# Kernel optimization log

Measured on AMD Instinct MI355X. Metric: run time of the kernel, lower is better.

The kernel has to match this reference:

```python
import jax, jax.numpy as jnp
import numpy as np

N = 100_000      # n_nodes
DEG = 32         # edge_threshold (fixed out-degree)
D = 64           # in_channels = out_channels, heads = 1
NEG_SLOPE = 0.2


def setup_inputs() -> dict:
    key = jax.random.key(0)
    k1, k2, k3, k4 = jax.random.split(key, 4)
    x = jax.random.normal(k1, (N, D), jnp.float32)
    # fixed-degree edge list with no self loops (offset in [1, N-1])
    src = jnp.repeat(jnp.arange(N, dtype=jnp.int64), DEG)
    off = jax.random.randint(k2, (N * DEG,), 1, N, dtype=jnp.int64)
    dst = (src + off) % N
    edge_index = jnp.stack([src, dst])  # [2, E]
    # glorot init as in the torch module
    stdv_w = float(np.sqrt(6.0 / (D + D)))
    weight = jax.random.uniform(k3, (D, D), jnp.float32, -stdv_w, stdv_w)
    stdv_a = float(np.sqrt(6.0 / (1 + 2 * D)))  # att is [1, heads=1, 2*D]
    att = jax.random.uniform(k4, (2 * D,), jnp.float32, -stdv_a, stdv_a)
    bias = jnp.zeros((D,), jnp.float32)
    return {"x": x, "edge_index": edge_index, "weight": weight, "att": att, "bias": bias}


def reference(x, edge_index, weight, att, bias):
    n, d = x.shape
    h = x @ weight                               # [N, D] (heads=1)
    # add self loops (inputs are constructed without self loops)
    loop = jnp.arange(n, dtype=edge_index.dtype)
    src = jnp.concatenate([edge_index[0], loop])  # message sources (x_j)
    dst = jnp.concatenate([edge_index[1], loop])  # aggregation targets (x_i)
    # GAT edge score: (cat([x_i, x_j]) * att).sum(-1) = h_i@a_i + h_j@a_j
    a_i, a_j = att[:d], att[d:]
    s_i = h @ a_i                                 # [N]
    s_j = h @ a_j                                 # [N]
    alpha = s_i[dst] + s_j[src]                   # [E+N]
    alpha = jnp.where(alpha > 0, alpha, NEG_SLOPE * alpha)  # leaky_relu
    # segment softmax over destination nodes (numerically stable)
    amax = jax.ops.segment_max(alpha, dst, num_segments=n)
    e = jnp.exp(alpha - amax[dst])
    denom = jax.ops.segment_sum(e, dst, num_segments=n)
    w = e / (denom[dst] + 1e-16)                  # [E+N]
    # weighted scatter-add aggregation of source features
    out = jax.ops.segment_sum(h[src] * w[:, None], dst, num_segments=n)  # [N, D]
    out = out + bias                              # head-mean is identity (heads=1)
    # dropout(p=0.5) is identity in eval mode; F.normalize (L2, dim=1, eps=1e-12)
    norm = jnp.linalg.norm(out, axis=1, keepdims=True)
    return out / jnp.maximum(norm, 1e-12)
```

## Files before the change

kernel.cpp:

```cpp
#include <hip/hip_runtime.h>
#include <math.h>

#define NEG_SLOPE 0.2f
#define PCHUNK 4096
#define NBINS_MAX 392
#define BIN_EDGE_CAP 8704

__device__ __forceinline__ unsigned pk_bf16x2(float a, float b) {
    unsigned ua = __float_as_uint(a);
    ua = (ua + 0x7FFFu + ((ua >> 16) & 1u)) >> 16;
    unsigned ub = __float_as_uint(b);
    ub = (ub + 0x7FFFu + ((ub >> 16) & 1u)) & 0xFFFF0000u;
    return ua | ub;
}

__global__ __launch_bounds__(256) void k_linear(const float* __restrict__ x,
        const float* __restrict__ W, const float* __restrict__ att,
        uint2* __restrict__ h16, float* __restrict__ si, float* __restrict__ sj,
        int n)
{
    int tid = threadIdx.x;
    int lane = tid & 63;
    int wv = tid >> 6;
    int q = lane >> 4;
    int f = lane & 15;

    const float4* W4 = (const float4*)W;
    float4 Wr[16];
#pragma unroll
    for (int kb = 0; kb < 16; ++kb)
        Wr[kb] = W4[(16 * q + kb) * 16 + f];

    const float4* att4 = (const float4*)att;
    float4 ai4 = att4[f];
    float4 aj4 = att4[16 + f];
    const float4* x4 = (const float4*)x;

    int row0 = (blockIdx.x * 4 + wv) * 8;
    for (int r = 0; r < 8; ++r) {
        int row = row0 + r;
        if (row >= n) break;
        size_t xb = (size_t)row * 16 + 4 * q;
        float4 xq0 = x4[xb + 0];
        float4 xq1 = x4[xb + 1];
        float4 xq2 = x4[xb + 2];
        float4 xq3 = x4[xb + 3];
        float4 acc = {0.f, 0.f, 0.f, 0.f};
#define LSTEP(xc, kb) { float4 w4 = Wr[kb]; \
        acc.x = fmaf((xc), w4.x, acc.x); acc.y = fmaf((xc), w4.y, acc.y); \
        acc.z = fmaf((xc), w4.z, acc.z); acc.w = fmaf((xc), w4.w, acc.w); }
        LSTEP(xq0.x, 0)  LSTEP(xq0.y, 1)  LSTEP(xq0.z, 2)  LSTEP(xq0.w, 3)
        LSTEP(xq1.x, 4)  LSTEP(xq1.y, 5)  LSTEP(xq1.z, 6)  LSTEP(xq1.w, 7)
        LSTEP(xq2.x, 8)  LSTEP(xq2.y, 9)  LSTEP(xq2.z, 10) LSTEP(xq2.w, 11)
        LSTEP(xq3.x, 12) LSTEP(xq3.y, 13) LSTEP(xq3.z, 14) LSTEP(xq3.w, 15)
#undef LSTEP
        acc.x += __shfl_xor(acc.x, 16); acc.x += __shfl_xor(acc.x, 32);
        acc.y += __shfl_xor(acc.y, 16); acc.y += __shfl_xor(acc.y, 32);
        acc.z += __shfl_xor(acc.z, 16); acc.z += __shfl_xor(acc.z, 32);
        acc.w += __shfl_xor(acc.w, 16); acc.w += __shfl_xor(acc.w, 32);

        if (q == 0) {
            uint2 p;
            p.x = pk_bf16x2(acc.x, acc.y);
            p.y = pk_bf16x2(acc.z, acc.w);
            h16[(size_t)row * 16 + f] = p;
        }

        float p = acc.x * ai4.x + acc.y * ai4.y + acc.z * ai4.z + acc.w * ai4.w;
        float pq = acc.x * aj4.x + acc.y * aj4.y + acc.z * aj4.z + acc.w * aj4.w;
#pragma unroll
        for (int o = 8; o >= 1; o >>= 1) {
            p += __shfl_xor(p, o);
            pq += __shfl_xor(pq, o);
        }
        if (lane == 0) { si[row] = p; sj[row] = pq; }
    }
}

__global__ __launch_bounds__(256) void k_hist(const int* __restrict__ dst, int E,
        int* __restrict__ hist_g, int NB, int nbins)
{
    __shared__ int hist[NBINS_MAX];
    int tid = threadIdx.x;
    int blk = blockIdx.x;
    int base = blk * PCHUNK;
    int cnt = E - base;
    if (cnt > PCHUNK) cnt = PCHUNK;
    for (int b = tid; b < nbins; b += 256) hist[b] = 0;
    __syncthreads();
    for (int i = tid; i < cnt; i += 256)
        atomicAdd(&hist[dst[base + i] >> 8], 1);
    __syncthreads();
    for (int b = tid; b < nbins; b += 256)
        hist_g[(size_t)b * NB + blk] = hist[b];
}

__global__ __launch_bounds__(256) void k_scan_a(int* __restrict__ data,
        int* __restrict__ bsum, int M)
{
    __shared__ int wsum[4];
    int tid = threadIdx.x;
    int lane = tid & 63;
    int wv = tid >> 6;
    int i0 = blockIdx.x * 1024 + tid * 4;
    int d0 = 0, d1 = 0, d2 = 0, d3 = 0;
    if (i0 + 3 < M) {
        int4 v = *(const int4*)(data + i0);
        d0 = v.x; d1 = v.y; d2 = v.z; d3 = v.w;
    } else {
        if (i0 + 0 < M) d0 = data[i0 + 0];
        if (i0 + 1 < M) d1 = data[i0 + 1];
        if (i0 + 2 < M) d2 = data[i0 + 2];
        if (i0 + 3 < M) d3 = data[i0 + 3];
    }
    int s = d0 + d1 + d2 + d3;
    int v = s;
#pragma unroll
    for (int o = 1; o < 64; o <<= 1) {
        int t = __shfl_up(v, o);
        if (lane >= o) v += t;
    }
    if (lane == 63) wsum[wv] = v;
    __syncthreads();
    int woff = 0;
    for (int w = 0; w < wv; ++w) woff += wsum[w];
    int ex = v - s + woff;
    if (i0 + 0 < M) data[i0 + 0] = ex; ex += d0;
    if (i0 + 1 < M) data[i0 + 1] = ex; ex += d1;
    if (i0 + 2 < M) data[i0 + 2] = ex; ex += d2;
    if (i0 + 3 < M) data[i0 + 3] = ex;
    if (tid == 255) bsum[blockIdx.x] = wsum[0] + wsum[1] + wsum[2] + wsum[3];
}

__global__ __launch_bounds__(256) void k_scan_b(const int* __restrict__ bsum,
        int* __restrict__ boff, int nb)
{
    __shared__ int wsum[4];
    int tid = threadIdx.x;
    int lane = tid & 63;
    int wv = tid >> 6;
    int t2 = tid * 2;
    int a = (t2 < nb) ? bsum[t2] : 0;
    int b = (t2 + 1 < nb) ? bsum[t2 + 1] : 0;
    int s = a + b;
    int v = s;
#pragma unroll
    for (int o = 1; o < 64; o <<= 1) {
        int t = __shfl_up(v, o);
        if (lane >= o) v += t;
    }
    if (lane == 63) wsum[wv] = v;
    __syncthreads();
    int woff = 0;
    for (int w = 0; w < wv; ++w) woff += wsum[w];
    int ex = v - s + woff;
    if (t2 < nb) boff[t2] = ex;
    if (t2 + 1 < nb) boff[t2 + 1] = ex + a;
}

__global__ __launch_bounds__(256) void k_scan_c(int* __restrict__ data,
        const int* __restrict__ boff, int M)
{
    int off = boff[blockIdx.x];
    int i0 = blockIdx.x * 1024 + threadIdx.x * 4;
#pragma unroll
    for (int k = 0; k < 4; ++k)
        if (i0 + k < M) data[i0 + k] += off;
}

__global__ __launch_bounds__(256) void k_part2(const int* __restrict__ src,
        const int* __restrict__ dst, int E,
        const int* __restrict__ hist_g, int NB, int nbins,
        unsigned* __restrict__ bin_edges)
{
    __shared__ unsigned stage[PCHUNK];
    __shared__ unsigned short sbin[PCHUNK];
    __shared__ int hist[NBINS_MAX];
    __shared__ int off[NBINS_MAX + 1];
    __shared__ int cur[NBINS_MAX];
    __shared__ int gbase[NBINS_MAX];
    __shared__ int wsum[4];

    int tid = threadIdx.x;
    int blk = blockIdx.x;
    int base = blk * PCHUNK;
    int cnt = E - base;
    if (cnt > PCHUNK) cnt = PCHUNK;

    for (int b = tid; b < nbins; b += 256) hist[b] = 0;
    __syncthreads();
    for (int i = tid; i < cnt; i += 256)
        atomicAdd(&hist[dst[base + i] >> 8], 1);
    __syncthreads();

    int lane = tid & 63;
    int wv = tid >> 6;
    int t2 = tid * 2;
    int a = (t2 < nbins) ? hist[t2] : 0;
    int b2 = (t2 + 1 < nbins) ? hist[t2 + 1] : 0;
    int s = a + b2;
    int v = s;
#pragma unroll
    for (int o = 1; o < 64; o <<= 1) {
        int t = __shfl_up(v, o);
        if (lane >= o) v += t;
    }
    if (lane == 63) wsum[wv] = v;
    __syncthreads();
    int woff = 0;
    for (int w = 0; w < wv; ++w) woff += wsum[w];
    int ex = v - s + woff;
    if (t2 <= nbins) off[t2] = ex;
    if (t2 + 1 <= nbins) off[t2 + 1] = ex + a;
    __syncthreads();

    for (int b = tid; b < nbins; b += 256) {
        cur[b] = off[b];
        gbase[b] = hist_g[(size_t)b * NB + blk];
    }
    __syncthreads();

    for (int i = tid; i < cnt; i += 256) {
        int e = base + i;
        int d = dst[e];
        int bb = d >> 8;
        int pos = atomicAdd(&cur[bb], 1);
        stage[pos] = ((unsigned)(d & 255) << 17) | (unsigned)src[e];
        sbin[pos] = (unsigned short)bb;
    }
    __syncthreads();
    for (int i = tid; i < cnt; i += 256) {
        int bb = sbin[i];
        bin_edges[gbase[bb] + (i - off[bb])] = stage[i];
    }
}

__global__ __launch_bounds__(256) void k_csr(const int* __restrict__ hist_g,
        int NB, int E, unsigned* __restrict__ bin_edges,
        int* __restrict__ row_start, int* __restrict__ deg, int n)
{
    __shared__ unsigned stage[BIN_EDGE_CAP];
    __shared__ int cnt256[256];
    __shared__ int off256[256];
    __shared__ int wsum[4];
    int b = blockIdx.x;
    int tid = threadIdx.x;
    int base = hist_g[(size_t)b * NB];
    int nxt = (b + 1 < (int)gridDim.x) ? hist_g[(size_t)(b + 1) * NB] : E;
    int cntE = nxt - base;
    if (cntE > BIN_EDGE_CAP) cntE = BIN_EDGE_CAP;

    for (int i = tid; i < cntE; i += 256) stage[i] = bin_edges[base + i];
    cnt256[tid] = 0;
    __syncthreads();
    for (int i = tid; i < cntE; i += 256)
        atomicAdd(&cnt256[stage[i] >> 17], 1);
    __syncthreads();

    int lane = tid & 63;
    int wv = tid >> 6;
    int s = cnt256[tid];
    int v = s;
#pragma unroll
    for (int o = 1; o < 64; o <<= 1) {
        int t = __shfl_up(v, o);
        if (lane >= o) v += t;
    }
    if (lane == 63) wsum[wv] = v;
    __syncthreads();
    int woff = 0;
    for (int w = 0; w < wv; ++w) woff += wsum[w];
    int ex = v - s + woff;
    off256[tid] = ex;

    int gd = b * 256 + tid;
    if (gd < n) {
        row_start[gd] = base + ex;
        deg[gd] = s;
    }
    __syncthreads();
    cnt256[tid] = ex;
    __syncthreads();
    for (int i = tid; i < cntE; i += 256) {
        unsigned pk = stage[i];
        int dl = (int)(pk >> 17);
        int pos = atomicAdd(&cnt256[dl], 1);
        bin_edges[base + pos] = pk & 0x1FFFFu;
    }
}

__global__ __launch_bounds__(256) void k_agg(const uint2* __restrict__ h16,
        const float* __restrict__ si, const float* __restrict__ sj,
        const int* __restrict__ row_start, const int* __restrict__ deg_arr,
        const unsigned* __restrict__ cols,
        const float* __restrict__ bias, float* __restrict__ out, int n)
{
    __shared__ int   sArr[4][132];
    __shared__ float wArr[4][132];
    int lane = threadIdx.x & 63;
    int wv = threadIdx.x >> 6;
    int d = blockIdx.x * 4 + wv;
    if (d >= n) return;

    int dg = deg_arr[d];
    if (dg > 128) dg = 128;
    int rs = row_start[d];
    float sid = si[d];

    int s0 = 0, s1 = 0;
    float a0 = -1e30f, a1 = -1e30f;
    if (lane < dg) {
        s0 = (int)cols[rs + lane];
        float t = sid + sj[s0];
        a0 = t > 0.f ? t : NEG_SLOPE * t;
    }
    if (lane + 64 < dg) {
        s1 = (int)cols[rs + lane + 64];
        float t = sid + sj[s1];
        a1 = t > 0.f ? t : NEG_SLOPE * t;
    }
    float tself = sid + sj[d];
    float aself = tself > 0.f ? tself : NEG_SLOPE * tself;

    float m = fmaxf(fmaxf(a0, a1), aself);
#pragma unroll
    for (int o = 32; o >= 1; o >>= 1) m = fmaxf(m, __shfl_xor(m, o));

    float e0 = (lane < dg) ? __expf(a0 - m) : 0.f;
    float e1 = (lane + 64 < dg) ? __expf(a1 - m) : 0.f;
    float eself = __expf(aself - m);

    float dsum = e0 + e1;
#pragma unroll
    for (int o = 32; o >= 1; o >>= 1) dsum += __shfl_xor(dsum, o);
    dsum += eself;

    if (lane < dg) { sArr[wv][lane] = s0; wArr[wv][lane] = e0; }
    if (lane + 64 < dg) { sArr[wv][lane + 64] = s1; wArr[wv][lane + 64] = e1; }
    if (lane == 0) { sArr[wv][dg] = d; wArr[wv][dg] = eself; }
    int cntAll = dg + 1;

    int q = lane >> 4;
    int f = lane & 15;
    float4 acc0 = {0.f, 0.f, 0.f, 0.f};
    float4 acc1 = {0.f, 0.f, 0.f, 0.f};
    int j = q;
    for (; j + 4 < cntAll; j += 8) {
        int   sA = sArr[wv][j];     float wA = wArr[wv][j];
        int   sB = sArr[wv][j + 4]; float wB = wArr[wv][j + 4];
        uint2 hA = h16[(size_t)sA * 16 + f];
        uint2 hB = h16[(size_t)sB * 16 + f];
        float ax = __uint_as_float(hA.x << 16);
        float ay = __uint_as_float(hA.x & 0xFFFF0000u);
        float az = __uint_as_float(hA.y << 16);
        float aw = __uint_as_float(hA.y & 0xFFFF0000u);
        float bx = __uint_as_float(hB.x << 16);
        float by = __uint_as_float(hB.x & 0xFFFF0000u);
        float bz = __uint_as_float(hB.y << 16);
        float bw = __uint_as_float(hB.y & 0xFFFF0000u);
        acc0.x = fmaf(wA, ax, acc0.x); acc0.y = fmaf(wA, ay, acc0.y);
        acc0.z = fmaf(wA, az, acc0.z); acc0.w = fmaf(wA, aw, acc0.w);
        acc1.x = fmaf(wB, bx, acc1.x); acc1.y = fmaf(wB, by, acc1.y);
        acc1.z = fmaf(wB, bz, acc1.z); acc1.w = fmaf(wB, bw, acc1.w);
    }
    if (j < cntAll) {
        int sA = sArr[wv][j]; float wA = wArr[wv][j];
        uint2 hA = h16[(size_t)sA * 16 + f];
        float ax = __uint_as_float(hA.x << 16);
        float ay = __uint_as_float(hA.x & 0xFFFF0000u);
        float az = __uint_as_float(hA.y << 16);
        float aw = __uint_as_float(hA.y & 0xFFFF0000u);
        acc0.x = fmaf(wA, ax, acc0.x); acc0.y = fmaf(wA, ay, acc0.y);
        acc0.z = fmaf(wA, az, acc0.z); acc0.w = fmaf(wA, aw, acc0.w);
    }
    acc0.x += acc1.x; acc0.y += acc1.y; acc0.z += acc1.z; acc0.w += acc1.w;

    acc0.x += __shfl_xor(acc0.x, 16); acc0.x += __shfl_xor(acc0.x, 32);
    acc0.y += __shfl_xor(acc0.y, 16); acc0.y += __shfl_xor(acc0.y, 32);
    acc0.z += __shfl_xor(acc0.z, 16); acc0.z += __shfl_xor(acc0.z, 32);
    acc0.w += __shfl_xor(acc0.w, 16); acc0.w += __shfl_xor(acc0.w, 32);

    float inv = 1.f / (dsum + 1e-16f);
    const float4* b4 = (const float4*)bias;
    float4 bb = b4[f];
    float4 o4;
    o4.x = acc0.x * inv + bb.x;
    o4.y = acc0.y * inv + bb.y;
    o4.z = acc0.z * inv + bb.z;
    o4.w = acc0.w * inv + bb.w;

    float nsq = o4.x * o4.x + o4.y * o4.y + o4.z * o4.z + o4.w * o4.w;
#pragma unroll
    for (int o = 8; o >= 1; o >>= 1) nsq += __shfl_xor(nsq, o);
    float rn = 1.f / fmaxf(sqrtf(nsq), 1e-12f);

    if (q == 0) {
        float4 res;
        res.x = o4.x * rn; res.y = o4.y * rn; res.z = o4.z * rn; res.w = o4.w * rn;
        ((float4*)out)[(size_t)d * 16 + f] = res;
    }
}

extern "C" void kernel_launch(void* const* d_in, const int* in_sizes, int n_in,
                              void* d_out, int out_size, void* d_ws, size_t ws_size,
                              hipStream_t stream)
{
    const float* x    = (const float*)d_in[0];
    const int*   ei   = (const int*)d_in[1];
    const float* W    = (const float*)d_in[2];
    const float* att  = (const float*)d_in[3];
    const float* bias = (const float*)d_in[4];
    float* out = (float*)d_out;

    int n = in_sizes[0] / 64;
    int E = in_sizes[1] / 2;
    const int* src = ei;
    const int* dst = ei + E;

    int nbins = (n + 255) >> 8;
    int NB = (E + PCHUNK - 1) / PCHUNK;
    int M = nbins * NB;
    int nsc = (M + 1023) / 1024;

    char* ws = (char*)d_ws;
#define CARVE(ptr, type, count) type* ptr = (type*)ws; \
        ws += (((size_t)(count) * sizeof(type)) + 255) & ~(size_t)255;
    CARVE(h16, uint2, (size_t)n * 16)
    CARVE(si, float, n)
    CARVE(sj, float, n)
    CARVE(row_start, int, n)
    CARVE(deg, int, n)
    CARVE(hist_g, int, M)
    CARVE(bsum, int, 512)
    CARVE(boff, int, 512)
    CARVE(bin_edges, unsigned, E)
#undef CARVE

    k_linear<<<(n + 31) / 32, 256, 0, stream>>>(x, W, att, h16, si, sj, n);
    k_hist<<<NB, 256, 0, stream>>>(dst, E, hist_g, NB, nbins);
    k_scan_a<<<nsc, 256, 0, stream>>>(hist_g, bsum, M);
    k_scan_b<<<1, 256, 0, stream>>>(bsum, boff, nsc);
    k_scan_c<<<nsc, 256, 0, stream>>>(hist_g, boff, M);
    k_part2<<<NB, 256, 0, stream>>>(src, dst, E, hist_g, NB, nbins, bin_edges);
    k_csr<<<nbins, 256, 0, stream>>>(hist_g, NB, E, bin_edges, row_start, deg, n);
    k_agg<<<(n + 3) / 4, 256, 0, stream>>>(h16, si, sj, row_start, deg, bin_edges, bias, out, n);
}
```

Measured before the change: 276.1 us.

## Halve bin width and scatter partition directly to global without LDS staging

Bins now cover 128 destination nodes instead of 256, which doubles the number of bins and the size of the histogram scan. The partition kernel drops its recomputed local histogram and scan plus the LDS staging, and writes each edge straight to its global slot through a shared-memory atomic cursor. The CSR kernel keeps each bin's edges in per-thread registers instead of a large LDS buffer, which should raise occupancy. The cost is uncoalesced global scatter writes in the partition step, a larger scan, and a silent cap of 20 edges per thread (5120 per bin) that could drop edges on skewed degree distributions.

```diff
diff --git a/kernel.cpp b/kernel.cpp
--- a/kernel.cpp
+++ b/kernel.cpp
@@ -3,8 +3,9 @@
 
 #define NEG_SLOPE 0.2f
 #define PCHUNK 4096
-#define NBINS_MAX 392
-#define BIN_EDGE_CAP 8704
+#define BIN_BITS 7
+#define NBINS_MAX 784
+#define CSR_MAX_PT 20
 
 __device__ __forceinline__ unsigned pk_bf16x2(float a, float b) {
     unsigned ua = __float_as_uint(a);
@@ -89,7 +90,7 @@
     for (int b = tid; b < nbins; b += 256) hist[b] = 0;
     __syncthreads();
     for (int i = tid; i < cnt; i += 256)
-        atomicAdd(&hist[dst[base + i] >> 8], 1);
+        atomicAdd(&hist[dst[base + i] >> BIN_BITS], 1);
     __syncthreads();
     for (int b = tid; b < nbins; b += 256)
         hist_g[(size_t)b * NB + blk] = hist[b];
@@ -139,10 +140,12 @@
     int tid = threadIdx.x;
     int lane = tid & 63;
     int wv = tid >> 6;
-    int t2 = tid * 2;
-    int a = (t2 < nb) ? bsum[t2] : 0;
-    int b = (t2 + 1 < nb) ? bsum[t2 + 1] : 0;
-    int s = a + b;
+    int t4 = tid * 4;
+    int a0 = (t4 + 0 < nb) ? bsum[t4 + 0] : 0;
+    int a1 = (t4 + 1 < nb) ? bsum[t4 + 1] : 0;
+    int a2 = (t4 + 2 < nb) ? bsum[t4 + 2] : 0;
+    int a3 = (t4 + 3 < nb) ? bsum[t4 + 3] : 0;
+    int s = a0 + a1 + a2 + a3;
     int v = s;
 #pragma unroll
     for (int o = 1; o < 64; o <<= 1) {
@@ -154,8 +157,10 @@
     int woff = 0;
     for (int w = 0; w < wv; ++w) woff += wsum[w];
     int ex = v - s + woff;
-    if (t2 < nb) boff[t2] = ex;
-    if (t2 + 1 < nb) boff[t2 + 1] = ex + a;
+    if (t4 + 0 < nb) boff[t4 + 0] = ex; ex += a0;
+    if (t4 + 1 < nb) boff[t4 + 1] = ex; ex += a1;
+    if (t4 + 2 < nb) boff[t4 + 2] = ex; ex += a2;
+    if (t4 + 3 < nb) boff[t4 + 3] = ex;
 }
 
 __global__ __launch_bounds__(256) void k_scan_c(int* __restrict__ data,
@@ -173,119 +178,76 @@
         const int* __restrict__ hist_g, int NB, int nbins,
         unsigned* __restrict__ bin_edges)
 {
-    __shared__ unsigned stage[PCHUNK];
-    __shared__ unsigned short sbin[PCHUNK];
-    __shared__ int hist[NBINS_MAX];
-    __shared__ int off[NBINS_MAX + 1];
     __shared__ int cur[NBINS_MAX];
-    __shared__ int gbase[NBINS_MAX];
-    __shared__ int wsum[4];
-
     int tid = threadIdx.x;
     int blk = blockIdx.x;
     int base = blk * PCHUNK;
     int cnt = E - base;
     if (cnt > PCHUNK) cnt = PCHUNK;
 
-    for (int b = tid; b < nbins; b += 256) hist[b] = 0;
-    __syncthreads();
-    for (int i = tid; i < cnt; i += 256)
-        atomicAdd(&hist[dst[base + i] >> 8], 1);
-    __syncthreads();
-
-    int lane = tid & 63;
-    int wv = tid >> 6;
-    int t2 = tid * 2;
-    int a = (t2 < nbins) ? hist[t2] : 0;
-    int b2 = (t2 + 1 < nbins) ? hist[t2 + 1] : 0;
-    int s = a + b2;
-    int v = s;
-#pragma unroll
-    for (int o = 1; o < 64; o <<= 1) {
-        int t = __shfl_up(v, o);
-        if (lane >= o) v += t;
-    }
-    if (lane == 63) wsum[wv] = v;
-    __syncthreads();
-    int woff = 0;
-    for (int w = 0; w < wv; ++w) woff += wsum[w];
-    int ex = v - s + woff;
-    if (t2 <= nbins) off[t2] = ex;
-    if (t2 + 1 <= nbins) off[t2 + 1] = ex + a;
-    __syncthreads();
-
-    for (int b = tid; b < nbins; b += 256) {
-        cur[b] = off[b];
-        gbase[b] = hist_g[(size_t)b * NB + blk];
-    }
+    for (int b = tid; b < nbins; b += 256)
+        cur[b] = hist_g[(size_t)b * NB + blk];
     __syncthreads();
 
     for (int i = tid; i < cnt; i += 256) {
         int e = base + i;
         int d = dst[e];
-        int bb = d >> 8;
+        int bb = d >> BIN_BITS;
         int pos = atomicAdd(&cur[bb], 1);
-        stage[pos] = ((unsigned)(d & 255) << 17) | (unsigned)src[e];
-        sbin[pos] = (unsigned short)bb;
-    }
-    __syncthreads();
-    for (int i = tid; i < cnt; i += 256) {
-        int bb = sbin[i];
-        bin_edges[gbase[bb] + (i - off[bb])] = stage[i];
+        bin_edges[pos] = ((unsigned)(d & 127) << 17) | (unsigned)src[e];
     }
 }
 
 __global__ __launch_bounds__(256) void k_csr(const int* __restrict__ hist_g,
         int NB, int E, unsigned* __restrict__ bin_edges,
-        int* __restrict__ row_start, int* __restrict__ deg, int n)
-{
-    __shared__ unsigned stage[BIN_EDGE_CAP];
-    __shared__ int cnt256[256];
-    __shared__ int off256[256];
-    __shared__ int wsum[4];
+        int* __restrict__ row_start, int* __restrict__ deg, int n, int nbins)
+{
+    __shared__ int cnt128[128];
+    __shared__ int off128[128];
     int b = blockIdx.x;
     int tid = threadIdx.x;
     int base = hist_g[(size_t)b * NB];
-    int nxt = (b + 1 < (int)gridDim.x) ? hist_g[(size_t)(b + 1) * NB] : E;
+    int nxt = (b + 1 < nbins) ? hist_g[(size_t)(b + 1) * NB] : E;
     int cntE = nxt - base;
-    if (cntE > BIN_EDGE_CAP) cntE = BIN_EDGE_CAP;
-
-    for (int i = tid; i < cntE; i += 256) stage[i] = bin_edges[base + i];
-    cnt256[tid] = 0;
-    __syncthreads();
-    for (int i = tid; i < cntE; i += 256)
-        atomicAdd(&cnt256[stage[i] >> 17], 1);
-    __syncthreads();
-
-    int lane = tid & 63;
-    int wv = tid >> 6;
-    int s = cnt256[tid];
-    int v = s;
-#pragma unroll
-    for (int o = 1; o < 64; o <<= 1) {
-        int t = __shfl_up(v, o);
-        if (lane >= o) v += t;
-    }
-    if (lane == 63) wsum[wv] = v;
-    __syncthreads();
-    int woff = 0;
-    for (int w = 0; w < wv; ++w) woff += wsum[w];
-    int ex = v - s + woff;
-    off256[tid] = ex;
-
-    int gd = b * 256 + tid;
-    if (gd < n) {
-        row_start[gd] = base + ex;
-        deg[gd] = s;
-    }
-    __syncthreads();
-    cnt256[tid] = ex;
+
+    unsigned pk[CSR_MAX_PT];
+    int nloc = 0;
+    if (tid < 128) cnt128[tid] = 0;
     __syncthreads();
     for (int i = tid; i < cntE; i += 256) {
-        unsigned pk = stage[i];
-        int dl = (int)(pk >> 17);
-        int pos = atomicAdd(&cnt256[dl], 1);
-        bin_edges[base + pos] = pk & 0x1FFFFu;
+        unsigned p = bin_edges[base + i];
+        if (nloc < CSR_MAX_PT) pk[nloc++] = p;
+        atomicAdd(&cnt128[p >> 17], 1);
+    }
+    __syncthreads();
+    if (tid < 64) {
+        int a = cnt128[2 * tid];
+        int bb = cnt128[2 * tid + 1];
+        int s = a + bb;
+        int v = s;
+#pragma unroll
+        for (int o = 1; o < 64; o <<= 1) {
+            int t = __shfl_up(v, o);
+            if (tid >= o) v += t;
+        }
+        int ex = v - s;
+        off128[2 * tid] = ex;
+        off128[2 * tid + 1] = ex + a;
+    }
+    __syncthreads();
+    int gd = b * 128 + tid;
+    if (tid < 128 && gd < n) {
+        row_start[gd] = base + off128[tid];
+        deg[gd] = cnt128[tid];
+    }
+    __syncthreads();
+    if (tid < 128) cnt128[tid] = off128[tid];
+    __syncthreads();
+    nloc = 0;
+    for (int i = tid; i < cntE; i += 256) {
+        unsigned p = pk[nloc++];
+        int pos = atomicAdd(&cnt128[p >> 17], 1);
+        bin_edges[base + pos] = p & 0x1FFFFu;
     }
 }
 
@@ -417,7 +379,7 @@
     const int* src = ei;
     const int* dst = ei + E;
 
-    int nbins = (n + 255) >> 8;
+    int nbins = (n + 127) >> BIN_BITS;
     int NB = (E + PCHUNK - 1) / PCHUNK;
     int M = nbins * NB;
     int nsc = (M + 1023) / 1024;
@@ -431,8 +393,8 @@
     CARVE(row_start, int, n)
     CARVE(deg, int, n)
     CARVE(hist_g, int, M)
-    CARVE(bsum, int, 512)
-    CARVE(boff, int, 512)
+    CARVE(bsum, int, 1024)
+    CARVE(boff, int, 1024)
     CARVE(bin_edges, unsigned, E)
 #undef CARVE
 
@@ -442,6 +404,6 @@
     k_scan_b<<<1, 256, 0, stream>>>(bsum, boff, nsc);
     k_scan_c<<<nsc, 256, 0, stream>>>(hist_g, boff, M);
     k_part2<<<NB, 256, 0, stream>>>(src, dst, E, hist_g, NB, nbins, bin_edges);
-    k_csr<<<nbins, 256, 0, stream>>>(hist_g, NB, E, bin_edges, row_start, deg, n);
+    k_csr<<<nbins, 256, 0, stream>>>(hist_g, NB, E, bin_edges, row_start, deg, n, nbins);
     k_agg<<<(n + 3) / 4, 256, 0, stream>>>(h16, si, sj, row_start, deg, bin_edges, bias, out, n);
 }
```

After: 317.0 us. 14.8% more time.
